# Optimization experiments

Measured on AMD Instinct MI355X. Metric: run time of the kernel, lower is better.

The kernel has to match this reference:

```python
import jax, jax.numpy as jnp
import numpy as np

B, S1, S2, D = 4, 64, 256, 256   # batch, nodes, time, model_dim
H = 8
HD = D // H
F = 1024
K = 3
EPS = 1e-5
NEG_SLOPE = 0.01


def setup_inputs() -> dict:
    key = jax.random.key(0)
    ks = jax.random.split(key, 16)
    s = 0.02
    return {
        "x": jax.random.normal(ks[0], (B, S1, S2, D), jnp.float32),
        "Wq": jax.random.normal(ks[1], (K, D, D), jnp.float32) * s,  # WIO conv1d kernel
        "bq": jnp.zeros((D,), jnp.float32),
        "Wk": jax.random.normal(ks[2], (K, D, D), jnp.float32) * s,
        "bk": jnp.zeros((D,), jnp.float32),
        "Wv": jax.random.normal(ks[3], (D, D), jnp.float32) * s,
        "bv": jnp.zeros((D,), jnp.float32),
        "Wo": jax.random.normal(ks[4], (D, D), jnp.float32) * s,
        "bo": jnp.zeros((D,), jnp.float32),
        "W1": jax.random.normal(ks[5], (D, F), jnp.float32) * s,
        "b1": jnp.zeros((F,), jnp.float32),
        "W2": jax.random.normal(ks[6], (F, D), jnp.float32) * s,
        "b2": jnp.zeros((D,), jnp.float32),
        "g1": jnp.ones((D,), jnp.float32),
        "be1": jnp.zeros((D,), jnp.float32),
        "g2": jnp.ones((D,), jnp.float32),
        "be2": jnp.zeros((D,), jnp.float32),
    }


def _conv_time(x, W, b):
    # x: [B, S1, S2, D]; conv over S2 (time) mixing all channels, padding K//2 (same length for odd K)
    xr = x.reshape(B * S1, S2, D)
    y = jax.lax.conv_general_dilated(
        xr, W, window_strides=(1,), padding=[(K // 2, K // 2)],
        dimension_numbers=("NWC", "WIO", "NWC"))
    return (y + b).reshape(B, S1, S2, D)


def _ln(x, g, b):
    mu = jnp.mean(x, axis=-1, keepdims=True)
    var = jnp.var(x, axis=-1, keepdims=True)
    return (x - mu) * jax.lax.rsqrt(var + EPS) * g + b


def reference(x, Wq, bq, Wk, bk, Wv, bv, Wo, bo, W1, b1, W2, b2, g1, be1, g2, be2):
    # --- attention (over time axis S2, per node S1) ---
    q = _conv_time(x, Wq, bq).reshape(B, S1, S2, H, HD)
    k = _conv_time(x, Wk, bk).reshape(B, S1, S2, H, HD)
    v = (x @ Wv + bv).reshape(B, S1, S2, H, HD)
    scores = jnp.einsum("bnthd,bnshd->bhnts", q, k) / jnp.sqrt(jnp.float32(HD))
    attn = jax.nn.softmax(scores, axis=-1)  # [B,H,S1,S2,S2]
    o = jnp.einsum("bhnts,bnshd->bnthd", attn, v).reshape(B, S1, S2, D)
    o = o @ Wo + bo
    # --- residual + LN + FFN (dropout=0 / eval) ---
    h = _ln(x + o, g1, be1)
    ff = jnp.where(h @ W1 + b1 > 0, h @ W1 + b1, NEG_SLOPE * (h @ W1 + b1))
    ff = ff @ W2 + b2
    return _ln(h + ff, g2, be2)
```

## Files before the change

### kernel.cpp

```cpp
#include <hip/hip_runtime.h>
#include <hip/hip_bf16.h>

#define B_ 4
#define S1_ 64
#define S2_ 256
#define D_ 256
#define H_ 8
#define HD_ 32
#define F_ 1024
#define EPS_ 1e-5f
#define NEG_ 0.01f

typedef __attribute__((ext_vector_type(8))) short bfrag;
typedef __attribute__((ext_vector_type(4))) float f32x4;
typedef __attribute__((ext_vector_type(8))) unsigned short us8;
typedef __attribute__((ext_vector_type(4))) unsigned short us4;

__device__ __forceinline__ unsigned short bf16rn(float f) {
    union { float f; unsigned int u; } c; c.f = f;
    unsigned int u = c.u;
    u = (u + 0x7FFFu + ((u >> 16) & 1u)) >> 16;
    return (unsigned short)u;
}
__device__ __forceinline__ float bf2f(unsigned short s) {
    union { unsigned int u; float f; } c; c.u = ((unsigned int)s) << 16;
    return c.f;
}

__device__ __forceinline__ void gload_lds16(const void* g, void* l) {
    __builtin_amdgcn_global_load_lds(
        (const __attribute__((address_space(1))) void*)g,
        (__attribute__((address_space(3))) void*)l,
        16, 0, 0);
}

__global__ __launch_bounds__(256) void k_xcast(
    const float* __restrict__ x, unsigned short* __restrict__ xb16)
{
    const size_t i = ((size_t)blockIdx.x * 256 + threadIdx.x) * 8;
    float4 f0 = *(const float4*)(x + i);
    float4 f1 = *(const float4*)(x + i + 4);
    us8 v;
    v[0] = bf16rn(f0.x); v[1] = bf16rn(f0.y); v[2] = bf16rn(f0.z); v[3] = bf16rn(f0.w);
    v[4] = bf16rn(f1.x); v[5] = bf16rn(f1.y); v[6] = bf16rn(f1.z); v[7] = bf16rn(f1.w);
    *(us8*)(xb16 + i) = v;
}

__global__ __launch_bounds__(256) void k_pack(
    const float* __restrict__ Wq, const float* __restrict__ Wk,
    const float* __restrict__ Wv, const float* __restrict__ Wo,
    const float* __restrict__ W1, const float* __restrict__ W2,
    unsigned short* __restrict__ Wq_pk, unsigned short* __restrict__ Wk_pk,
    unsigned short* __restrict__ Wv_pk, unsigned short* __restrict__ Wo_pk,
    unsigned short* __restrict__ W1_pk, unsigned short* __restrict__ W2_pk)
{
    const int blk = blockIdx.x;
    const float* src; unsigned short* dst; int Ntot = 256, n0 = 0, k0;
    if (blk < 12)      { src = Wq; k0 = blk * 64;        dst = Wq_pk + (size_t)blk * 16384; }
    else if (blk < 24) { src = Wk; k0 = (blk - 12) * 64; dst = Wk_pk + (size_t)(blk - 12) * 16384; }
    else if (blk < 28) { src = Wv; k0 = (blk - 24) * 64; dst = Wv_pk + (size_t)(blk - 24) * 16384; }
    else if (blk < 44) {
        const int i = blk - 28; const int p = i >> 2, c = i & 3;
        src = W1; Ntot = 1024; n0 = p * 256; k0 = c * 64;
        dst = W1_pk + (size_t)i * 16384;
    }
    else if (blk < 60) { src = W2; k0 = (blk - 44) * 64; dst = W2_pk + (size_t)(blk - 44) * 16384; }
    else               { src = Wo; k0 = (blk - 60) * 64; dst = Wo_pk + (size_t)(blk - 60) * 16384; }

    const int tid = threadIdx.x;
    for (int j = 0; j < 8; ++j) {
        const int fi = j * 256 + tid;
        const int lane = fi & 63;
        const int t2 = fi >> 6;
        const int nt = t2 >> 1, kk = t2 & 1;
        const int col = lane & 15, q4 = lane >> 4;
        const int n = n0 + nt * 16 + col;
        const int kbase = k0 + kk * 32 + q4 * 8;
        us8 v;
        #pragma unroll
        for (int e = 0; e < 8; ++e)
            v[e] = bf16rn(src[(size_t)(kbase + e) * Ntot + n]);
        *(us8*)(dst + (size_t)fi * 8) = v;
    }
}

__global__ __launch_bounds__(512, 4) void k_qkv_gemm(
    const unsigned short* __restrict__ xb16,
    const unsigned short* __restrict__ Wq_pk, const unsigned short* __restrict__ Wk_pk,
    const unsigned short* __restrict__ Wv_pk,
    const float* __restrict__ bq, const float* __restrict__ bk,
    const float* __restrict__ bv,
    unsigned short* __restrict__ qpk, unsigned short* __restrict__ kpk,
    unsigned short* __restrict__ vpk)
{
    __shared__ __align__(16) unsigned short As[128][72];
    __shared__ __align__(16) unsigned short Bs[16384];

    const int tid = threadIdx.x, w = tid >> 6, lane = tid & 63;
    const int col = lane & 15, q4 = lane >> 4;
    const int wr = w >> 2, wc = w & 3;
    const int y = blockIdx.y;
    const int bn = blockIdx.x >> 1, half = blockIdx.x & 1, t0 = half * 128;
    const int nch = (y == 2) ? 4 : 12;
    const unsigned short* Wpk = (y == 0) ? Wq_pk : (y == 1) ? Wk_pk : Wv_pk;

    f32x4 acc[4][4];
    #pragma unroll
    for (int m = 0; m < 4; ++m)
        #pragma unroll
        for (int n = 0; n < 4; ++n)
            acc[m][n] = (f32x4){0.f, 0.f, 0.f, 0.f};

    const int arow = tid >> 2, aq = (tid & 3) * 16;

    for (int c = 0; c < nch; ++c) {
        const int s  = (y == 2) ? 1 : (c >> 2);
        const int c0 = (y == 2) ? (c * 64) : ((c & 3) * 64);

        const int trow = t0 + s - 1 + arow;
        const bool ok = (trow >= 0) && (trow < 256);
        const int trc = ok ? trow : (trow < 0 ? 0 : 255);
        const unsigned short* ap = xb16 + ((size_t)bn * 256 + trc) * 256 + c0 + aq;
        us8 av[2];
        #pragma unroll
        for (int j = 0; j < 2; ++j)
            av[j] = *(const us8*)(ap + j * 8);

        const char* wb = (const char*)(Wpk + (size_t)c * 16384);
        #pragma unroll
        for (int r = 0; r < 4; ++r) {
            const int boff = (r * 8 + w) * 1024;
            gload_lds16(wb + boff + lane * 16, ((char*)Bs) + boff);
        }

        #pragma unroll
        for (int j = 0; j < 2; ++j) {
            us8 v = av[j];
            if (!ok) v = (us8){0, 0, 0, 0, 0, 0, 0, 0};
            *(us8*)&As[arow][aq + j * 8] = v;
        }
        __syncthreads();

        #pragma unroll
        for (int kk = 0; kk < 2; ++kk) {
            bfrag a[4], b[4];
            #pragma unroll
            for (int m = 0; m < 4; ++m)
                a[m] = *(const bfrag*)&As[wr * 64 + m * 16 + col][kk * 32 + q4 * 8];
            #pragma unroll
            for (int n = 0; n < 4; ++n)
                b[n] = *(const bfrag*)&Bs[(((wc * 4 + n) * 2 + kk) * 64 + lane) * 8];
            #pragma unroll
            for (int n = 0; n < 4; ++n)
                #pragma unroll
                for (int m = 0; m < 4; ++m)
                    acc[m][n] = __builtin_amdgcn_mfma_f32_16x16x32_bf16(a[m], b[n], acc[m][n], 0, 0, 0);
        }
        __syncthreads();
    }

    if (y == 2) {
        #pragma unroll
        for (int n = 0; n < 4; ++n) {
            const int nn = wc * 64 + n * 16 + col;
            const int hh = nn >> 5, d = nn & 31;
            const float bb = bv[nn];
            #pragma unroll
            for (int m = 0; m < 4; ++m) {
                const int s0 = t0 + wr * 64 + m * 16 + q4 * 4;
                us4 pk;
                #pragma unroll
                for (int r = 0; r < 4; ++r)
                    pk[r] = bf16rn(acc[m][n][r] + bb);
                const int kc = (s0 >> 5) & 7, q3 = (s0 >> 3) & 3, e0 = s0 & 7;
                *(us4*)(vpk + (((((size_t)bn * 8 + hh) * 8 + kc) * 2 + (d >> 4)) * 64
                               + (d & 15) + 16 * q3) * 8 + e0) = pk;
            }
        }
    } else {
        unsigned short* dst = (y == 0) ? qpk : kpk;
        const float* bias = (y == 0) ? bq : bk;
        #pragma unroll
        for (int n = 0; n < 4; ++n) {
            const int nn = wc * 64 + n * 16 + col;
            const int hh = nn >> 5, hd = nn & 31;
            const float bb = bias[nn];
            #pragma unroll
            for (int m = 0; m < 4; ++m) {
                const int tile = (t0 >> 4) + wr * 4 + m;
                unsigned short* dp = dst
                    + ((((size_t)bn * 8 + hh) * 16 + tile) * 64 + 16 * (hd >> 3)) * 8
                    + (hd & 7);
                #pragma unroll
                for (int r = 0; r < 4; ++r)
                    dp[(q4 * 4 + r) * 8] = bf16rn(acc[m][n][r] + bb);
            }
        }
    }
}

__global__ __launch_bounds__(256) void k_attn_mfma(
    const unsigned short* __restrict__ qpk, const unsigned short* __restrict__ kpk,
    const unsigned short* __restrict__ vpk, unsigned short* __restrict__ ob)
{
    __shared__ __align__(16) unsigned short KsL[8192];
    __shared__ __align__(16) unsigned short Pw[4][16][264];

    const int bn   = blockIdx.x;
    const int h    = blockIdx.y;
    const int tid  = threadIdx.x;
    const int w    = tid >> 6;
    const int lane = tid & 63;
    const int col  = lane & 15;
    const int q4   = lane >> 4;
    const size_t bhi = (size_t)bn * 8 + h;
    const size_t obase = (size_t)bn * S2_ * D_ + h * HD_;
    const unsigned short* qbase = qpk + bhi * 8192;
    const unsigned short* vbase = vpk + bhi * 8192;
    const float SCL2E = 0.17677669529663687f * 1.4426950408889634f;

    {
        const char* kb = (const char*)(kpk + bhi * 8192);
        #pragma unroll
        for (int r = 0; r < 4; ++r) {
            const int fi = r * 4 + w;
            gload_lds16(kb + fi * 1024 + lane * 16, ((char*)KsL) + fi * 1024);
        }
    }
    __syncthreads();

    for (int mt = 0; mt < 4; ++mt) {
        bfrag qa = *(const bfrag*)(qbase + ((size_t)(w * 4 + mt) * 64 + lane) * 8);

        f32x4 sc[16];
        #pragma unroll
        for (int nt = 0; nt < 16; ++nt) {
            bfrag kf = *(const bfrag*)&KsL[(nt * 64 + lane) * 8];
            f32x4 z = {0.f, 0.f, 0.f, 0.f};
            sc[nt] = __builtin_amdgcn_mfma_f32_16x16x32_bf16(qa, kf, z, 0, 0, 0);
        }

        float mx[4] = {-1e30f, -1e30f, -1e30f, -1e30f};
        #pragma unroll
        for (int nt = 0; nt < 16; ++nt)
            #pragma unroll
            for (int r = 0; r < 4; ++r) {
                sc[nt][r] *= SCL2E;
                mx[r] = fmaxf(mx[r], sc[nt][r]);
            }
        #pragma unroll
        for (int r = 0; r < 4; ++r) {
            mx[r] = fmaxf(mx[r], __shfl_xor(mx[r], 1));
            mx[r] = fmaxf(mx[r], __shfl_xor(mx[r], 2));
            mx[r] = fmaxf(mx[r], __shfl_xor(mx[r], 4));
            mx[r] = fmaxf(mx[r], __shfl_xor(mx[r], 8));
        }
        float l[4] = {0.f, 0.f, 0.f, 0.f};
        #pragma unroll
        for (int nt = 0; nt < 16; ++nt)
            #pragma unroll
            for (int r = 0; r < 4; ++r) {
                const float e = exp2f(sc[nt][r] - mx[r]);
                sc[nt][r] = e;
                l[r] += e;
            }
        #pragma unroll
        for (int r = 0; r < 4; ++r) {
            l[r] += __shfl_xor(l[r], 1);
            l[r] += __shfl_xor(l[r], 2);
            l[r] += __shfl_xor(l[r], 4);
            l[r] += __shfl_xor(l[r], 8);
        }

        #pragma unroll
        for (int nt = 0; nt < 16; ++nt)
            #pragma unroll
            for (int r = 0; r < 4; ++r)
                Pw[w][q4 * 4 + r][nt * 16 + col] = bf16rn(sc[nt][r]);

        f32x4 oacc[2];
        oacc[0] = (f32x4){0.f, 0.f, 0.f, 0.f};
        oacc[1] = (f32x4){0.f, 0.f, 0.f, 0.f};
        #pragma unroll
        for (int kc = 0; kc < 8; ++kc) {
            bfrag pa = *(const bfrag*)&Pw[w][col][kc * 32 + q4 * 8];
            bfrag v0 = *(const bfrag*)(vbase + ((size_t)(kc * 2 + 0) * 64 + lane) * 8);
            bfrag v1 = *(const bfrag*)(vbase + ((size_t)(kc * 2 + 1) * 64 + lane) * 8);
            oacc[0] = __builtin_amdgcn_mfma_f32_16x16x32_bf16(pa, v0, oacc[0], 0, 0, 0);
            oacc[1] = __builtin_amdgcn_mfma_f32_16x16x32_bf16(pa, v1, oacc[1], 0, 0, 0);
        }

        const int r0w = w * 64;
        float inv[4];
        #pragma unroll
        for (int r = 0; r < 4; ++r) inv[r] = 1.f / l[r];
        #pragma unroll
        for (int dt = 0; dt < 2; ++dt)
            #pragma unroll
            for (int r = 0; r < 4; ++r)
                ob[obase + (size_t)(r0w + mt * 16 + q4 * 4 + r) * D_ + dt * 16 + col]
                    = bf16rn(oacc[dt][r] * inv[r]);
    }
}

__global__ __launch_bounds__(256) void k_oproj_gemm(
    const unsigned short* __restrict__ ob,
    const unsigned short* __restrict__ Wo_pk, const float* __restrict__ bo,
    const float* __restrict__ x,
    const float* __restrict__ g1, const float* __restrict__ be1,
    unsigned short* __restrict__ hb)
{
    __shared__ __align__(16) unsigned short As[128][72];
    __shared__ __align__(16) unsigned short Bs[16384];
    __shared__ float red[128][2][2];

    const int tid = threadIdx.x, w = tid >> 6, lane = tid & 63;
    const int col = lane & 15, q4 = lane >> 4;
    const int wr = w >> 1, wc = w & 1;
    const size_t tok0 = (size_t)blockIdx.x * 128;

    f32x4 acc[4][8];
    #pragma unroll
    for (int m = 0; m < 4; ++m)
        #pragma unroll
        for (int n = 0; n < 8; ++n)
            acc[m][n] = (f32x4){0.f, 0.f, 0.f, 0.f};

    const int arow = tid >> 1, ahalf = (tid & 1) * 32;

    for (int c = 0; c < 4; ++c) {
        const unsigned short* ap = ob + (tok0 + arow) * D_ + c * 64 + ahalf;
        us8 av[4];
        #pragma unroll
        for (int j = 0; j < 4; ++j)
            av[j] = *(const us8*)(ap + j * 8);

        const char* wb = (const char*)(Wo_pk + (size_t)c * 16384);
        #pragma unroll
        for (int r = 0; r < 8; ++r) {
            const int boff = (r * 4 + w) * 1024;
            gload_lds16(wb + boff + lane * 16, ((char*)Bs) + boff);
        }

        #pragma unroll
        for (int j = 0; j < 4; ++j)
            *(us8*)&As[arow][ahalf + j * 8] = av[j];
        __syncthreads();

        #pragma unroll
        for (int kk = 0; kk < 2; ++kk) {
            bfrag a[4], b[8];
            #pragma unroll
            for (int m = 0; m < 4; ++m)
                a[m] = *(const bfrag*)&As[wr * 64 + m * 16 + col][kk * 32 + q4 * 8];
            #pragma unroll
            for (int n = 0; n < 8; ++n)
                b[n] = *(const bfrag*)&Bs[(((wc * 8 + n) * 2 + kk) * 64 + lane) * 8];
            #pragma unroll
            for (int n = 0; n < 8; ++n)
                #pragma unroll
                for (int m = 0; m < 4; ++m)
                    acc[m][n] = __builtin_amdgcn_mfma_f32_16x16x32_bf16(a[m], b[n], acc[m][n], 0, 0, 0);
        }
        __syncthreads();
    }

    float bov[8];
    #pragma unroll
    for (int n = 0; n < 8; ++n)
        bov[n] = bo[wc * 128 + n * 16 + col];

    float s[4][4], s2[4][4];
    #pragma unroll
    for (int m = 0; m < 4; ++m)
        #pragma unroll
        for (int r = 0; r < 4; ++r) { s[m][r] = 0.f; s2[m][r] = 0.f; }

    #pragma unroll
    for (int m = 0; m < 4; ++m)
        #pragma unroll
        for (int r = 0; r < 4; ++r) {
            const size_t row = tok0 + wr * 64 + m * 16 + q4 * 4 + r;
            #pragma unroll
            for (int n = 0; n < 8; ++n) {
                const int nn = wc * 128 + n * 16 + col;
                const float yv = acc[m][n][r] + bov[n] + x[row * D_ + nn];
                acc[m][n][r] = yv;
                s[m][r] += yv;
                s2[m][r] = fmaf(yv, yv, s2[m][r]);
            }
        }

    #pragma unroll
    for (int m = 0; m < 4; ++m)
        #pragma unroll
        for (int r = 0; r < 4; ++r) {
            #pragma unroll
            for (int d = 1; d < 16; d <<= 1) {
                s[m][r]  += __shfl_xor(s[m][r],  d);
                s2[m][r] += __shfl_xor(s2[m][r], d);
            }
        }

    if (col == 0) {
        #pragma unroll
        for (int m = 0; m < 4; ++m)
            #pragma unroll
            for (int r = 0; r < 4; ++r) {
                const int rl = wr * 64 + m * 16 + q4 * 4 + r;
                red[rl][wc][0] = s[m][r];
                red[rl][wc][1] = s2[m][r];
            }
    }
    __syncthreads();

    float mu[4][4], rs[4][4];
    #pragma unroll
    for (int m = 0; m < 4; ++m)
        #pragma unroll
        for (int r = 0; r < 4; ++r) {
            const int rl = wr * 64 + m * 16 + q4 * 4 + r;
            const float ts  = red[rl][0][0] + red[rl][1][0];
            const float ts2 = red[rl][0][1] + red[rl][1][1];
            const float m_  = ts * (1.f / 256.f);
            mu[m][r] = m_;
            rs[m][r] = rsqrtf(ts2 * (1.f / 256.f) - m_ * m_ + EPS_);
        }

    #pragma unroll
    for (int n = 0; n < 8; ++n) {
        const int nn = wc * 128 + n * 16 + col;
        const float gv = g1[nn], bev = be1[nn];
        #pragma unroll
        for (int m = 0; m < 4; ++m)
            #pragma unroll
            for (int r = 0; r < 4; ++r) {
                const size_t row = tok0 + wr * 64 + m * 16 + q4 * 4 + r;
                hb[row * D_ + nn] = bf16rn((acc[m][n][r] - mu[m][r]) * rs[m][r] * gv + bev);
            }
    }
}

__global__ __launch_bounds__(256) void k_ffn1_gemm(
    const unsigned short* __restrict__ hb,
    const unsigned short* __restrict__ W1_pk, const float* __restrict__ b1,
    unsigned short* __restrict__ ff)
{
    __shared__ __align__(16) unsigned short As[128][72];
    __shared__ __align__(16) unsigned short Bs[16384];

    const int tid = threadIdx.x, w = tid >> 6, lane = tid & 63;
    const int col = lane & 15, q4 = lane >> 4;
    const int wr = w >> 1, wc = w & 1;
    const size_t tok0 = (size_t)blockIdx.x * 128;
    const int y = blockIdx.y;
    const unsigned short* Wpk = W1_pk + (size_t)y * 4 * 16384;

    f32x4 acc[4][8];
    #pragma unroll
    for (int m = 0; m < 4; ++m)
        #pragma unroll
        for (int n = 0; n < 8; ++n)
            acc[m][n] = (f32x4){0.f, 0.f, 0.f, 0.f};

    const int arow = tid >> 1, ahalf = (tid & 1) * 32;

    for (int c = 0; c < 4; ++c) {
        const unsigned short* ap = hb + (tok0 + arow) * D_ + c * 64 + ahalf;
        us8 av[4];
        #pragma unroll
        for (int j = 0; j < 4; ++j)
            av[j] = *(const us8*)(ap + j * 8);

        const char* wb = (const char*)(Wpk + (size_t)c * 16384);
        #pragma unroll
        for (int r = 0; r < 8; ++r) {
            const int boff = (r * 4 + w) * 1024;
            gload_lds16(wb + boff + lane * 16, ((char*)Bs) + boff);
        }

        #pragma unroll
        for (int j = 0; j < 4; ++j)
            *(us8*)&As[arow][ahalf + j * 8] = av[j];
        __syncthreads();

        #pragma unroll
        for (int kk = 0; kk < 2; ++kk) {
            bfrag a[4], b[8];
            #pragma unroll
            for (int m = 0; m < 4; ++m)
                a[m] = *(const bfrag*)&As[wr * 64 + m * 16 + col][kk * 32 + q4 * 8];
            #pragma unroll
            for (int n = 0; n < 8; ++n)
                b[n] = *(const bfrag*)&Bs[(((wc * 8 + n) * 2 + kk) * 64 + lane) * 8];
            #pragma unroll
            for (int n = 0; n < 8; ++n)
                #pragma unroll
                for (int m = 0; m < 4; ++m)
                    acc[m][n] = __builtin_amdgcn_mfma_f32_16x16x32_bf16(a[m], b[n], acc[m][n], 0, 0, 0);
        }
        __syncthreads();
    }

    #pragma unroll
    for (int n = 0; n < 8; ++n) {
        const int nglob = y * 256 + wc * 128 + n * 16 + col;
        const float bb = b1[nglob];
        #pragma unroll
        for (int m = 0; m < 4; ++m)
            #pragma unroll
            for (int r = 0; r < 4; ++r) {
                float v = acc[m][n][r] + bb;
                v = (v > 0.f) ? v : NEG_ * v;
                ff[(tok0 + wr * 64 + m * 16 + q4 * 4 + r) * (size_t)F_ + nglob] = bf16rn(v);
            }
    }
}

__global__ __launch_bounds__(256) void k_ffn2_gemm(
    const unsigned short* __restrict__ ff,
    const unsigned short* __restrict__ W2_pk, const float* __restrict__ b2,
    const unsigned short* __restrict__ hb,
    const float* __restrict__ g2, const float* __restrict__ be2,
    float* __restrict__ out)
{
    __shared__ __align__(16) unsigned short As[128][72];
    __shared__ __align__(16) unsigned short Bs[16384];
    __shared__ float red[128][2][2];

    const int tid = threadIdx.x, w = tid >> 6, lane = tid & 63;
    const int col = lane & 15, q4 = lane >> 4;
    const int wr = w >> 1, wc = w & 1;
    const size_t tok0 = (size_t)blockIdx.x * 128;

    f32x4 acc[4][8];
    #pragma unroll
    for (int m = 0; m < 4; ++m)
        #pragma unroll
        for (int n = 0; n < 8; ++n)
            acc[m][n] = (f32x4){0.f, 0.f, 0.f, 0.f};

    const int arow = tid >> 1, ahalf = (tid & 1) * 32;

    for (int c = 0; c < 16; ++c) {
        const unsigned short* ap = ff + (tok0 + arow) * (size_t)F_ + c * 64 + ahalf;
        us8 av[4];
        #pragma unroll
        for (int j = 0; j < 4; ++j)
            av[j] = *(const us8*)(ap + j * 8);

        const char* wb = (const char*)(W2_pk + (size_t)c * 16384);
        #pragma unroll
        for (int r = 0; r < 8; ++r) {
            const int boff = (r * 4 + w) * 1024;
            gload_lds16(wb + boff + lane * 16, ((char*)Bs) + boff);
        }

        #pragma unroll
        for (int j = 0; j < 4; ++j)
            *(us8*)&As[arow][ahalf + j * 8] = av[j];
        __syncthreads();

        #pragma unroll
        for (int kk = 0; kk < 2; ++kk) {
            bfrag a[4], b[8];
            #pragma unroll
            for (int m = 0; m < 4; ++m)
                a[m] = *(const bfrag*)&As[wr * 64 + m * 16 + col][kk * 32 + q4 * 8];
            #pragma unroll
            for (int n = 0; n < 8; ++n)
                b[n] = *(const bfrag*)&Bs[(((wc * 8 + n) * 2 + kk) * 64 + lane) * 8];
            #pragma unroll
            for (int n = 0; n < 8; ++n)
                #pragma unroll
                for (int m = 0; m < 4; ++m)
                    acc[m][n] = __builtin_amdgcn_mfma_f32_16x16x32_bf16(a[m], b[n], acc[m][n], 0, 0, 0);
        }
        __syncthreads();
    }

    float b2v[8];
    #pragma unroll
    for (int n = 0; n < 8; ++n)
        b2v[n] = b2[wc * 128 + n * 16 + col];

    float s[4][4], s2[4][4];
    #pragma unroll
    for (int m = 0; m < 4; ++m)
        #pragma unroll
        for (int r = 0; r < 4; ++r) { s[m][r] = 0.f; s2[m][r] = 0.f; }

    #pragma unroll
    for (int m = 0; m < 4; ++m)
        #pragma unroll
        for (int r = 0; r < 4; ++r) {
            const size_t row = tok0 + wr * 64 + m * 16 + q4 * 4 + r;
            #pragma unroll
            for (int n = 0; n < 8; ++n) {
                const int nn = wc * 128 + n * 16 + col;
                const float yv = acc[m][n][r] + b2v[n] + bf2f(hb[row * D_ + nn]);
                acc[m][n][r] = yv;
                s[m][r] += yv;
                s2[m][r] = fmaf(yv, yv, s2[m][r]);
            }
        }

    #pragma unroll
    for (int m = 0; m < 4; ++m)
        #pragma unroll
        for (int r = 0; r < 4; ++r) {
            #pragma unroll
            for (int d = 1; d < 16; d <<= 1) {
                s[m][r]  += __shfl_xor(s[m][r],  d);
                s2[m][r] += __shfl_xor(s2[m][r], d);
            }
        }

    if (col == 0) {
        #pragma unroll
        for (int m = 0; m < 4; ++m)
            #pragma unroll
            for (int r = 0; r < 4; ++r) {
                const int rl = wr * 64 + m * 16 + q4 * 4 + r;
                red[rl][wc][0] = s[m][r];
                red[rl][wc][1] = s2[m][r];
            }
    }
    __syncthreads();

    float mu[4][4], rs[4][4];
    #pragma unroll
    for (int m = 0; m < 4; ++m)
        #pragma unroll
        for (int r = 0; r < 4; ++r) {
            const int rl = wr * 64 + m * 16 + q4 * 4 + r;
            const float ts  = red[rl][0][0] + red[rl][1][0];
            const float ts2 = red[rl][0][1] + red[rl][1][1];
            const float m_  = ts * (1.f / 256.f);
            mu[m][r] = m_;
            rs[m][r] = rsqrtf(ts2 * (1.f / 256.f) - m_ * m_ + EPS_);
        }

    #pragma unroll
    for (int n = 0; n < 8; ++n) {
        const int nn = wc * 128 + n * 16 + col;
        const float gv = g2[nn], bev = be2[nn];
        #pragma unroll
        for (int m = 0; m < 4; ++m)
            #pragma unroll
            for (int r = 0; r < 4; ++r) {
                const size_t row = tok0 + wr * 64 + m * 16 + q4 * 4 + r;
                out[row * D_ + nn] = (acc[m][n][r] - mu[m][r]) * rs[m][r] * gv + bev;
            }
    }
}

extern "C" void kernel_launch(void* const* d_in, const int* in_sizes, int n_in,
                              void* d_out, int out_size, void* d_ws, size_t ws_size,
                              hipStream_t stream)
{
    const float* x   = (const float*)d_in[0];
    const float* Wq  = (const float*)d_in[1];
    const float* bq  = (const float*)d_in[2];
    const float* Wk  = (const float*)d_in[3];
    const float* bk  = (const float*)d_in[4];
    const float* Wv  = (const float*)d_in[5];
    const float* bv  = (const float*)d_in[6];
    const float* Wo  = (const float*)d_in[7];
    const float* bo  = (const float*)d_in[8];
    const float* W1  = (const float*)d_in[9];
    const float* b1  = (const float*)d_in[10];
    const float* W2  = (const float*)d_in[11];
    const float* b2  = (const float*)d_in[12];
    const float* g1  = (const float*)d_in[13];
    const float* be1 = (const float*)d_in[14];
    const float* g2  = (const float*)d_in[15];
    const float* be2 = (const float*)d_in[16];
    float* out = (float*)d_out;

    const size_t N = (size_t)B_ * S1_ * S2_ * D_;

    unsigned short* qpk = (unsigned short*)d_ws;
    unsigned short* kpk = qpk + N;
    unsigned short* vpk = kpk + N;
    unsigned short* ob  = vpk + N;
    float*          h   = (float*)(ob + N);
    unsigned short* Wq_pk = (unsigned short*)(h + N);
    unsigned short* Wk_pk = Wq_pk + (size_t)12 * 16384;
    unsigned short* Wv_pk = Wk_pk + (size_t)12 * 16384;
    unsigned short* Wo_pk = Wv_pk + (size_t)4 * 16384;
    unsigned short* W1_pk = Wo_pk + (size_t)4 * 16384;
    unsigned short* W2_pk = W1_pk + (size_t)16 * 16384;
    const size_t need = (size_t)(W2_pk + (size_t)16 * 16384 - (unsigned short*)d_ws) * 2;
    if (ws_size < need) return;

    unsigned short* xb16 = (unsigned short*)h;
    unsigned short* hb   = (unsigned short*)h;
    unsigned short* ff   = qpk;

    k_xcast     <<<dim3((unsigned)(N / 2048)), 256, 0, stream>>>(x, xb16);
    k_pack      <<<dim3(64), 256, 0, stream>>>(Wq, Wk, Wv, Wo, W1, W2,
                    Wq_pk, Wk_pk, Wv_pk, Wo_pk, W1_pk, W2_pk);
    k_qkv_gemm  <<<dim3(512, 3), 512, 0, stream>>>(
                    xb16, Wq_pk, Wk_pk, Wv_pk, bq, bk, bv, qpk, kpk, vpk);
    k_attn_mfma <<<dim3(B_ * S1_, H_), 256, 0, stream>>>(qpk, kpk, vpk, ob);
    k_oproj_gemm<<<dim3(512), 256, 0, stream>>>(
                    ob, Wo_pk, bo, x, g1, be1, hb);
    k_ffn1_gemm <<<dim3(512, 4), 256, 0, stream>>>(hb, W1_pk, b1, ff);
    k_ffn2_gemm <<<dim3(512), 256, 0, stream>>>(ff, W2_pk, b2, hb, g2, be2, out);
}
```

Measured before the change: 548.3 us.

## Recompute QK scores in two passes, drop K LDS staging, raise occupancy

The attention kernel no longer keeps all 16 score tiles in registers. It runs QK^T twice, once to find the row max and once to compute the exponentials and write P to shared memory. K is now read straight from global memory instead of being staged in LDS, which removes a shared buffer and a block barrier. launch_bounds is raised to ask for 4 blocks per CU. The aim is lower register and LDS pressure for higher occupancy, at the cost of doubling the QK MFMA work and repeating global K loads.

```diff
diff --git a/kernel.cpp b/kernel.cpp
--- a/kernel.cpp
+++ b/kernel.cpp
@@ -199,11 +199,10 @@
     }
 }
 
-__global__ __launch_bounds__(256) void k_attn_mfma(
+__global__ __launch_bounds__(256, 4) void k_attn_mfma(
     const unsigned short* __restrict__ qpk, const unsigned short* __restrict__ kpk,
     const unsigned short* __restrict__ vpk, unsigned short* __restrict__ ob)
 {
-    __shared__ __align__(16) unsigned short KsL[8192];
     __shared__ __align__(16) unsigned short Pw[4][16][264];
 
     const int bn   = blockIdx.x;
@@ -216,54 +215,45 @@
     const size_t bhi = (size_t)bn * 8 + h;
     const size_t obase = (size_t)bn * S2_ * D_ + h * HD_;
     const unsigned short* qbase = qpk + bhi * 8192;
+    const unsigned short* kbase = kpk + bhi * 8192;
     const unsigned short* vbase = vpk + bhi * 8192;
     const float SCL2E = 0.17677669529663687f * 1.4426950408889634f;
 
-    {
-        const char* kb = (const char*)(kpk + bhi * 8192);
-        #pragma unroll
-        for (int r = 0; r < 4; ++r) {
-            const int fi = r * 4 + w;
-            gload_lds16(kb + fi * 1024 + lane * 16, ((char*)KsL) + fi * 1024);
-        }
-    }
-    __syncthreads();
-
     for (int mt = 0; mt < 4; ++mt) {
         bfrag qa = *(const bfrag*)(qbase + ((size_t)(w * 4 + mt) * 64 + lane) * 8);
 
-        f32x4 sc[16];
+        float mx[4] = {-1e30f, -1e30f, -1e30f, -1e30f};
         #pragma unroll
         for (int nt = 0; nt < 16; ++nt) {
-            bfrag kf = *(const bfrag*)&KsL[(nt * 64 + lane) * 8];
+            bfrag kf = *(const bfrag*)(kbase + ((size_t)(nt * 64 + lane)) * 8);
             f32x4 z = {0.f, 0.f, 0.f, 0.f};
-            sc[nt] = __builtin_amdgcn_mfma_f32_16x16x32_bf16(qa, kf, z, 0, 0, 0);
-        }
-
-        float mx[4] = {-1e30f, -1e30f, -1e30f, -1e30f};
-        #pragma unroll
-        for (int nt = 0; nt < 16; ++nt)
-            #pragma unroll
-            for (int r = 0; r < 4; ++r) {
-                sc[nt][r] *= SCL2E;
-                mx[r] = fmaxf(mx[r], sc[nt][r]);
-            }
+            f32x4 s = __builtin_amdgcn_mfma_f32_16x16x32_bf16(qa, kf, z, 0, 0, 0);
+            #pragma unroll
+            for (int r = 0; r < 4; ++r)
+                mx[r] = fmaxf(mx[r], s[r]);
+        }
         #pragma unroll
         for (int r = 0; r < 4; ++r) {
             mx[r] = fmaxf(mx[r], __shfl_xor(mx[r], 1));
             mx[r] = fmaxf(mx[r], __shfl_xor(mx[r], 2));
             mx[r] = fmaxf(mx[r], __shfl_xor(mx[r], 4));
             mx[r] = fmaxf(mx[r], __shfl_xor(mx[r], 8));
-        }
+            mx[r] *= SCL2E;
+        }
+
         float l[4] = {0.f, 0.f, 0.f, 0.f};
         #pragma unroll
-        for (int nt = 0; nt < 16; ++nt)
+        for (int nt = 0; nt < 16; ++nt) {
+            bfrag kf = *(const bfrag*)(kbase + ((size_t)(nt * 64 + lane)) * 8);
+            f32x4 z = {0.f, 0.f, 0.f, 0.f};
+            f32x4 s = __builtin_amdgcn_mfma_f32_16x16x32_bf16(qa, kf, z, 0, 0, 0);
             #pragma unroll
             for (int r = 0; r < 4; ++r) {
-                const float e = exp2f(sc[nt][r] - mx[r]);
-                sc[nt][r] = e;
+                const float e = exp2f(fmaf(s[r], SCL2E, -mx[r]));
                 l[r] += e;
-            }
+                Pw[w][q4 * 4 + r][nt * 16 + col] = bf16rn(e);
+            }
+        }
         #pragma unroll
         for (int r = 0; r < 4; ++r) {
             l[r] += __shfl_xor(l[r], 1);
@@ -271,12 +261,6 @@
             l[r] += __shfl_xor(l[r], 4);
             l[r] += __shfl_xor(l[r], 8);
         }
-
-        #pragma unroll
-        for (int nt = 0; nt < 16; ++nt)
-            #pragma unroll
-            for (int r = 0; r < 4; ++r)
-                Pw[w][q4 * 4 + r][nt * 16 + col] = bf16rn(sc[nt][r]);
 
         f32x4 oacc[2];
         oacc[0] = (f32x4){0.f, 0.f, 0.f, 0.f};
```

New measurement: 627.2 us. +14.4%, slower.
